# Kernel optimization log

Measured on AMD Instinct MI355X. Metric: run time of the kernel, lower is better.

The kernel has to match this reference:

```python
import jax, jax.numpy as jnp
import numpy as np

B, S, D_MODEL, H, N_LAYERS = 4, 1024, 512, 8, 6
DEPTH = D_MODEL // H


def setup_inputs() -> dict:
    key = jax.random.key(0)
    ks = jax.random.split(key, 16)
    sc = 1.0 / np.sqrt(D_MODEL)
    inp = {
        'v': jax.random.normal(ks[0], (B, S, D_MODEL), jnp.float32),
        'q': jax.random.normal(ks[1], (B, S, D_MODEL), jnp.float32),
        'k': jax.random.normal(ks[2], (B, S, D_MODEL), jnp.float32),
        'wq_w': jax.random.normal(ks[3], (D_MODEL, D_MODEL), jnp.float32) * sc,
        'wq_b': jnp.zeros((D_MODEL,), jnp.float32),
        'wk_w': jax.random.normal(ks[4], (D_MODEL, D_MODEL), jnp.float32) * sc,
        'wk_b': jnp.zeros((D_MODEL,), jnp.float32),
        'wv_w': jax.random.normal(ks[5], (D_MODEL, D_MODEL), jnp.float32) * sc,
        'wv_b': jnp.zeros((D_MODEL,), jnp.float32),
        'wo_w': jax.random.normal(ks[6], (D_MODEL, D_MODEL), jnp.float32) * sc,
        'wo_b': jnp.zeros((D_MODEL,), jnp.float32),
        'aug_hb': jax.random.uniform(ks[7], (N_LAYERS, 1), jnp.float32),
        'aug_pi': jax.random.uniform(ks[8], (N_LAYERS, 1), jnp.float32),
        'aug_at': jax.random.uniform(ks[9], (N_LAYERS, 1), jnp.float32),
        'table_hb': jax.random.normal(ks[10], (S, S), jnp.float32),
        'table_pi': jax.random.normal(ks[11], (S, S), jnp.float32),
        'mask': (jax.random.uniform(ks[12], (B, 1, S, S)) < 0.1).astype(jnp.float32),
        'block_num': 0,
    }
    return inp


def _split_heads(x):
    # (B, S, d_model) -> (B, H, S, depth)
    return x.reshape(B, S, H, DEPTH).transpose(0, 2, 1, 3)


def reference(v, q, k, wq_w, wq_b, wk_w, wk_b, wv_w, wv_b, wo_w, wo_b,
              aug_hb, aug_pi, aug_at, table_hb, table_pi, mask, block_num):
    qh = _split_heads(q @ wq_w + wq_b)
    kh = _split_heads(k @ wk_w + wk_b)
    vh = _split_heads(v @ wv_w + wv_b)

    # NOTE: original call site swaps q/k positionally, so scores = K . Q^T
    scores = jnp.einsum('bhid,bhjd->bhij', kh, qh)  # (B,H,S,S)
    dk = jnp.float32(DEPTH)
    logits = scores / jnp.sqrt(dk) + mask * (-1e9)

    # per-layer table augmentation (tables broadcast over batch & heads)
    logits = logits * aug_at[block_num] \
        + aug_hb[block_num] * table_hb \
        + aug_pi[block_num] * table_pi

    # joint softmax over axes (2, 3)
    m = jnp.max(logits, axis=(2, 3), keepdims=True)
    e = jnp.exp(logits - m)
    attn = e / jnp.sum(e, axis=(2, 3), keepdims=True)

    ctx = jnp.einsum('bhij,bhjd->bhid', attn, vh)          # (B,H,S,depth)
    ctx = ctx.transpose(0, 2, 1, 3).reshape(B, S, D_MODEL)  # concat heads
    out = ctx @ wo_w + wo_b
    return out, attn
```

## Files before the change

### kernel.cpp

```cpp
#include <hip/hip_runtime.h>
#include <math.h>

#define NS 1024
#define DM 512
#define NH 8
#define DEPTH 64

#define OFF_QH   0
#define OFF_KH   2097152
#define OFF_VH   4194304
#define OFF_CTX0 0
#define OFF_CTX1 2097152
#define OFF_PART 6291456

#define ESW(row, col) ((col) ^ ((((row) >> 3) & 7) << 2))

#define LO_SCALE 2048.0f
#define LO_INV   (1.0f/2048.0f)
#define F16_MIN_NORM 6.1035156e-5f
#define ASCALE   4096.0f
#define AUNSCALE (1.0f/4096.0f)

typedef float f4 __attribute__((ext_vector_type(4)));
typedef _Float16 h8 __attribute__((ext_vector_type(8)));
typedef _Float16 h4 __attribute__((ext_vector_type(4)));
typedef float f32x4v __attribute__((ext_vector_type(4)));

#define SPLIT1(x, hi_e, lo_e) {                                          \
    const float x_ = (x);                                                \
    _Float16 t = (fabsf(x_) >= F16_MIN_NORM) ? (_Float16)x_ : (_Float16)0.f; \
    hi_e = t;                                                            \
    lo_e = (_Float16)((x_ - (float)t) * LO_SCALE);                       \
}

#define SPLIT8(u0, u1, hi, lo) {                                         \
    SPLIT1(u0.x, hi[0], lo[0]) SPLIT1(u0.y, hi[1], lo[1])                \
    SPLIT1(u0.z, hi[2], lo[2]) SPLIT1(u0.w, hi[3], lo[3])                \
    SPLIT1(u1.x, hi[4], lo[4]) SPLIT1(u1.y, hi[5], lo[5])                \
    SPLIT1(u1.z, hi[6], lo[6]) SPLIT1(u1.w, hi[7], lo[7])                \
}

#define MM(accH, accM, a_h, a_l, b_h, b_l) {                                   \
    accH = __builtin_amdgcn_mfma_f32_16x16x32_f16(a_h, b_h, accH, 0, 0, 0);    \
    accM = __builtin_amdgcn_mfma_f32_16x16x32_f16(a_l, b_h, accM, 0, 0, 0);    \
    accM = __builtin_amdgcn_mfma_f32_16x16x32_f16(a_h, b_l, accM, 0, 0, 0);    \
}
#define MM1(acc, a_h, a_l, b_h, b_l) {                                         \
    acc = __builtin_amdgcn_mfma_f32_16x16x32_f16(a_h, b_h, acc, 0, 0, 0);      \
    acc = __builtin_amdgcn_mfma_f32_16x16x32_f16(a_l, b_h, acc, 0, 0, 0);      \
    acc = __builtin_amdgcn_mfma_f32_16x16x32_f16(a_h, b_l, acc, 0, 0, 0);      \
}

__device__ __forceinline__ void prep_one(
    const float* __restrict__ W, _Float16* __restrict__ whi,
    _Float16* __restrict__ wlo, int g)
{
    const int kk = g >> 7;
    const int n  = (g & 127) * 4;
    const float4 f = *(const float4*)(W + (size_t)kk * DM + n);
    const int gbase = (kk >> 3) * 128 + (kk & 7);
    #define PREP1(val, nn) {                                             \
        const int a_ = ((nn) >> 4) * 8192 + gbase + ((nn) & 15) * 8;     \
        _Float16 h_; _Float16 l_;                                        \
        SPLIT1(val, h_, l_)                                              \
        whi[a_] = h_; wlo[a_] = l_;                                      \
    }
    PREP1(f.x, n + 0) PREP1(f.y, n + 1) PREP1(f.z, n + 2) PREP1(f.w, n + 3)
    #undef PREP1
}

__global__ __launch_bounds__(256) void k_prep_qkv(
    const float* __restrict__ wq, const float* __restrict__ wk,
    const float* __restrict__ wv, float* __restrict__ attn)
{
    const int w = blockIdx.y;
    const float* W = (w == 0) ? wq : (w == 1) ? wk : wv;
    _Float16* base = (_Float16*)attn + (size_t)w * 524288;
    prep_one(W, base, base + 262144, blockIdx.x * 256 + threadIdx.x);
}

__global__ __launch_bounds__(256) void k_prep_wo(
    const float* __restrict__ wo, float* __restrict__ ws)
{
    _Float16* base = (_Float16*)(ws + OFF_VH);
    prep_one(wo, base, base + 262144, blockIdx.x * 256 + threadIdx.x);
}

__global__ __launch_bounds__(256) void k_prep_aux(
    const float* __restrict__ mask, const float* __restrict__ t_hb,
    const float* __restrict__ t_pi,
    const float* __restrict__ aug_hb, const float* __restrict__ aug_pi,
    const float* __restrict__ aug_at, const int* __restrict__ bnum,
    float* __restrict__ outp)
{
    const int g = blockIdx.x * 256 + threadIdx.x;
    const size_t e0 = (size_t)g * 4;
    const size_t t0 = e0 & (size_t)(NS*NS - 1);
    const int bn = bnum[0];
    const float at = aug_at[bn], hb = aug_hb[bn], pi = aug_pi[bn];
    const float m_at = -1e9f * at;
    const f4 m4 = *(const f4*)(mask + e0);
    const f4 th = *(const f4*)(t_hb + t0);
    const f4 tp = *(const f4*)(t_pi + t0);
    h4 o;
    float a;
    a = fmaf(m4.x, m_at, fmaf(hb, th.x, pi*tp.x)); if (a < -60000.f) a = -60000.f; o[0] = (_Float16)a;
    a = fmaf(m4.y, m_at, fmaf(hb, th.y, pi*tp.y)); if (a < -60000.f) a = -60000.f; o[1] = (_Float16)a;
    a = fmaf(m4.z, m_at, fmaf(hb, th.z, pi*tp.z)); if (a < -60000.f) a = -60000.f; o[2] = (_Float16)a;
    a = fmaf(m4.w, m_at, fmaf(hb, th.w, pi*tp.w)); if (a < -60000.f) a = -60000.f; o[3] = (_Float16)a;
    *(h4*)((_Float16*)outp + e0) = o;
}

__global__ __launch_bounds__(256, 3) void k_proj(
    const float* __restrict__ q, const float* __restrict__ k, const float* __restrict__ v,
    const float* __restrict__ bq, const float* __restrict__ bk, const float* __restrict__ bv,
    float* __restrict__ ws, const float* __restrict__ attn)
{
    const float *X, *bias; int wsel;
    if (blockIdx.z == 0)      { X=q; bias=bq; wsel=0; }
    else if (blockIdx.z == 1) { X=k; bias=bk; wsel=1; }
    else                      { X=v; bias=bv; wsel=2; }
    float* outf = ws + OFF_VH;
    _Float16* outh = (_Float16*)(ws + (wsel == 0 ? OFF_QH : OFF_KH));

    const int f = blockIdx.x + (blockIdx.y << 3);
    const int n0 = (f >> 5) * 64, m0 = (f & 31) * 128;
    const int tid = threadIdx.x, l = tid & 63, w = tid >> 6;
    const int lr = l & 15, lg = l >> 4;

    const _Float16* whi = (const _Float16*)attn + (size_t)wsel * 524288;
    const _Float16* wlo = whi + 262144;
    const float* ap0 = X + (size_t)(m0 + w*32 + lr) * DM + lg*8;
    const float* ap1 = ap0 + (size_t)16 * DM;
    const _Float16* bh_base = whi + (size_t)(n0 >> 4) * 8192 + lg*128 + lr*8;
    const _Float16* bl_base = wlo + (size_t)(n0 >> 4) * 8192 + lg*128 + lr*8;

    f32x4v aH00 = 0, aH01 = 0, aH02 = 0, aH03 = 0;
    f32x4v aH10 = 0, aH11 = 0, aH12 = 0, aH13 = 0;
    f32x4v aM00 = 0, aM01 = 0, aM02 = 0, aM03 = 0;
    f32x4v aM10 = 0, aM11 = 0, aM12 = 0, aM13 = 0;

    #pragma unroll 1
    for (int kb = 0; kb < DM; kb += 32) {
        h8 ah0, al0, ah1, al1;
        {
            const float4 u0 = *(const float4*)(ap0 + kb);
            const float4 u1 = *(const float4*)(ap0 + kb + 4);
            SPLIT8(u0, u1, ah0, al0);
            const float4 v0 = *(const float4*)(ap1 + kb);
            const float4 v1 = *(const float4*)(ap1 + kb + 4);
            SPLIT8(v0, v1, ah1, al1);
        }
        const int boff = kb * 16;
        const h8 bh0 = *(const h8*)(bh_base + boff);
        const h8 bh1 = *(const h8*)(bh_base + boff + 8192);
        const h8 bh2 = *(const h8*)(bh_base + boff + 16384);
        const h8 bh3 = *(const h8*)(bh_base + boff + 24576);
        const h8 bl0 = *(const h8*)(bl_base + boff);
        const h8 bl1 = *(const h8*)(bl_base + boff + 8192);
        const h8 bl2 = *(const h8*)(bl_base + boff + 16384);
        const h8 bl3 = *(const h8*)(bl_base + boff + 24576);

        MM(aH00, aM00, ah0, al0, bh0, bl0) MM(aH01, aM01, ah0, al0, bh1, bl1)
        MM(aH02, aM02, ah0, al0, bh2, bl2) MM(aH03, aM03, ah0, al0, bh3, bl3)
        MM(aH10, aM10, ah1, al1, bh0, bl0) MM(aH11, aM11, ah1, al1, bh1, bl1)
        MM(aH12, aM12, ah1, al1, bh2, bl2) MM(aH13, aM13, ah1, al1, bh3, bl3)
    }

    const int h = n0 >> 6;
    #define STORE_TILE(accH, accM, nt, mt) {                                 \
        const int n = n0 + (nt)*16 + lr;                                     \
        const float bsv = bias[n];                                           \
        const int d = n & 63;                                                \
        const int mbase = m0 + w*32 + (mt)*16 + lg*4;                        \
        _Pragma("unroll")                                                    \
        for (int r = 0; r < 4; ++r) {                                        \
            const int m = mbase + r;                                         \
            const int bb = m >> 10, s = m & 1023;                            \
            const float val = fmaf(accM[r], LO_INV, accH[r]) + bsv;          \
            if (wsel == 2) {                                                 \
                outf[(((size_t)(bb*NH + h))*NS + s)*DEPTH + d] = val;        \
            } else {                                                         \
                _Float16* p = outh + (size_t)(bb*NH + h)*131072              \
                                   + (size_t)s*64 + d;                       \
                const _Float16 hi_ = (_Float16)val;                          \
                p[0]     = hi_;                                              \
                p[65536] = (_Float16)(val - (float)hi_);                     \
            }                                                                \
        }                                                                    \
    }
    STORE_TILE(aH00, aM00, 0, 0) STORE_TILE(aH10, aM10, 0, 1)
    STORE_TILE(aH01, aM01, 1, 0) STORE_TILE(aH11, aM11, 1, 1)
    STORE_TILE(aH02, aM02, 2, 0) STORE_TILE(aH12, aM12, 2, 1)
    STORE_TILE(aH03, aM03, 3, 0) STORE_TILE(aH13, aM13, 3, 1)
    #undef STORE_TILE
}

__global__ __launch_bounds__(256, 4) void k_score(
    float* __restrict__ ws,
    const _Float16* __restrict__ aux,
    const float* __restrict__ aug_at, const int* __restrict__ bnum,
    float* __restrict__ attn)
{
    __shared__ float wred[4];
    const int bh = blockIdx.z, b = bh >> 3;
    const int f = blockIdx.x + (blockIdx.y << 3);
    const int r = f & 7, qq = f >> 3;
    const int it = ((r & 1) << 2) | (qq & 3);
    const int jt_ = ((r >> 1) << 1) | (qq >> 2);
    const int i0 = it * 128, j0 = jt_ * 128;
    const _Float16* kb_ = (const _Float16*)(ws + OFF_KH) + (size_t)bh * 131072;
    const _Float16* qb_ = (const _Float16*)(ws + OFF_QH) + (size_t)bh * 131072;
    const int tid = threadIdx.x, l = tid & 63, w = tid >> 6;
    const int lr = l & 15, lg = l >> 4;

    const _Float16* ka = kb_ + (size_t)(i0 + w*32 + lr) * 64 + lg*8;
    const _Float16* qa = qb_ + (size_t)(j0 + lr) * 64 + lg*8;

    f32x4v acc[2][8] = {};
    #pragma unroll
    for (int d0 = 0; d0 < 2; ++d0) {
        const int dd = d0 * 32;
        const h8 ah0 = *(const h8*)(ka + dd);
        const h8 al0 = *(const h8*)(ka + dd + 65536);
        const h8 ah1 = *(const h8*)(ka + dd + 16*64);
        const h8 al1 = *(const h8*)(ka + dd + 16*64 + 65536);
        #pragma unroll
        for (int jt = 0; jt < 8; ++jt) {
            const h8 bhf = *(const h8*)(qa + dd + jt*16*64);
            const h8 blf = *(const h8*)(qa + dd + jt*16*64 + 65536);
            MM1(acc[0][jt], ah0, al0, bhf, blf)
            MM1(acc[1][jt], ah1, al1, bhf, blf)
        }
    }

    const int bn = bnum[0];
    const float sc_at = 0.125f * aug_at[bn];
    float local = 0.f;
    #pragma unroll
    for (int it2 = 0; it2 < 2; ++it2) {
        #pragma unroll
        for (int rr = 0; rr < 4; ++rr) {
            const int gi = i0 + w*32 + it2*16 + lg*4 + rr;
            const size_t xrow = ((size_t)b*NS + gi)*NS;
            const size_t arow = ((size_t)bh*NS + gi)*NS;
            #pragma unroll
            for (int jt = 0; jt < 8; ++jt) {
                const int gj = j0 + jt*16 + lr;
                const float xv = (float)aux[xrow + gj];
                const float e = __expf(fmaf(acc[it2][jt][rr], sc_at, xv));
                attn[arow + gj] = e;
                local += e;
            }
        }
    }
    #pragma unroll
    for (int o = 32; o > 0; o >>= 1) local += __shfl_down(local, o);
    if ((tid & 63) == 0) wred[tid >> 6] = local;
    __syncthreads();
    if (tid == 0)
        ws[OFF_PART + bh*64 + it*8 + jt_] =
            (wred[0] + wred[1]) + (wred[2] + wred[3]);
}

__global__ __launch_bounds__(256, 4) void k_pv(
    float* __restrict__ ws, float* __restrict__ attn)
{
    __shared__ float Es[64][68];
    __shared__ float Vs[64][68];
    __shared__ float s_inv;
    const int F = blockIdx.x + (blockIdx.y << 1) + (blockIdx.z << 5);
    const int r = F & 7, s = F >> 3;
    const int bh = (r << 2) | (s & 3);
    const int w = s >> 2;
    const int i0 = (w >> 1) * 64;
    const int jh = w & 1;
    const int b = bh >> 3, h = bh & 7;
    const float* vh = ws + OFF_VH + (size_t)bh*NS*DEPTH;
    float* pctx = ws + (jh ? OFF_CTX1 : OFF_CTX0);
    const int tid = threadIdx.x, tx = tid & 15, ty = tid >> 4;
    const int er_ = tid >> 4, ec4 = tid & 15;

    if (tid < 64) {
        float vsum = ws[OFF_PART + bh*64 + tid];
        #pragma unroll
        for (int o = 32; o > 0; o >>= 1) vsum += __shfl_down(vsum, o);
        if (tid == 0) s_inv = 1.0f / vsum;
    }
    __syncthreads();
    const float inv = s_inv;

    float acc[4][4] = {};
    for (int jt = 0; jt < 8; ++jt) {
        const int j0 = jh*512 + jt*64;
        #pragma unroll
        for (int l = 0; l < 4; ++l) {
            const int rr = er_ + l*16;
            float* ap = attn + ((size_t)bh*NS + i0 + rr)*NS + j0 + ec4*4;
            f4 e4 = *(const f4*)ap;
            e4 *= inv;
            *(f4*)ap = e4;
            Es[ec4*4+0][ESW(ec4*4+0, rr)] = e4.x;
            Es[ec4*4+1][ESW(ec4*4+1, rr)] = e4.y;
            Es[ec4*4+2][ESW(ec4*4+2, rr)] = e4.z;
            Es[ec4*4+3][ESW(ec4*4+3, rr)] = e4.w;
            *(float4*)&Vs[rr][ec4*4] = *(const float4*)(vh + (size_t)(j0+rr)*DEPTH + ec4*4);
        }
        __syncthreads();
        #pragma unroll
        for (int jj = 0; jj < 64; ++jj) {
            const float4 a  = *(const float4*)&Es[jj][ESW(jj, ty*4)];
            const float4 vv = *(const float4*)&Vs[jj][tx*4];
            const float av[4] = {a.x,a.y,a.z,a.w};
            const float vw[4] = {vv.x,vv.y,vv.z,vv.w};
            #pragma unroll
            for (int i = 0; i < 4; ++i)
                #pragma unroll
                for (int d = 0; d < 4; ++d)
                    acc[i][d] = fmaf(av[i], vw[d], acc[i][d]);
        }
        __syncthreads();
    }
    #pragma unroll
    for (int i = 0; i < 4; ++i) {
        const int gi = i0 + ty*4 + i;
        float4 o;
        o.x = acc[i][0]; o.y = acc[i][1]; o.z = acc[i][2]; o.w = acc[i][3];
        *(float4*)(pctx + ((size_t)b*NS + gi)*DM + h*DEPTH + tx*4) = o;
    }
}

__global__ __launch_bounds__(256, 3) void k_out(
    const float* __restrict__ wsc, const float* __restrict__ bo,
    float* __restrict__ outp)
{
    const int f = blockIdx.x + (blockIdx.y << 3);
    const int n0 = (f >> 5) * 64, m0 = (f & 31) * 128;
    const int tid = threadIdx.x, l = tid & 63, w = tid >> 6;
    const int lr = l & 15, lg = l >> 4;

    const _Float16* whi = (const _Float16*)(wsc + OFF_VH);
    const _Float16* wlo = whi + 262144;
    const float* ap0 = wsc + OFF_CTX0 + (size_t)(m0 + w*32 + lr) * DM + lg*8;
    const float* ap1 = wsc + OFF_CTX1 + (size_t)(m0 + w*32 + lr) * DM + lg*8;
    const _Float16* bh_base = whi + (size_t)(n0 >> 4) * 8192 + lg*128 + lr*8;
    const _Float16* bl_base = wlo + (size_t)(n0 >> 4) * 8192 + lg*128 + lr*8;

    f32x4v aH00 = 0, aH01 = 0, aH02 = 0, aH03 = 0;
    f32x4v aH10 = 0, aH11 = 0, aH12 = 0, aH13 = 0;
    f32x4v aM00 = 0, aM01 = 0, aM02 = 0, aM03 = 0;
    f32x4v aM10 = 0, aM11 = 0, aM12 = 0, aM13 = 0;

    #pragma unroll 1
    for (int kb = 0; kb < DM; kb += 32) {
        h8 ah0, al0, ah1, al1;
        {
            float4 u0 = *(const float4*)(ap0 + kb);
            float4 u1 = *(const float4*)(ap0 + kb + 4);
            const float4 c0 = *(const float4*)(ap1 + kb);
            const float4 c1 = *(const float4*)(ap1 + kb + 4);
            u0.x=(u0.x+c0.x)*ASCALE; u0.y=(u0.y+c0.y)*ASCALE;
            u0.z=(u0.z+c0.z)*ASCALE; u0.w=(u0.w+c0.w)*ASCALE;
            u1.x=(u1.x+c1.x)*ASCALE; u1.y=(u1.y+c1.y)*ASCALE;
            u1.z=(u1.z+c1.z)*ASCALE; u1.w=(u1.w+c1.w)*ASCALE;
            SPLIT8(u0, u1, ah0, al0);
            float4 v0 = *(const float4*)(ap0 + (size_t)16*DM + kb);
            float4 v1 = *(const float4*)(ap0 + (size_t)16*DM + kb + 4);
            const float4 d0 = *(const float4*)(ap1 + (size_t)16*DM + kb);
            const float4 d1 = *(const float4*)(ap1 + (size_t)16*DM + kb + 4);
            v0.x=(v0.x+d0.x)*ASCALE; v0.y=(v0.y+d0.y)*ASCALE;
            v0.z=(v0.z+d0.z)*ASCALE; v0.w=(v0.w+d0.w)*ASCALE;
            v1.x=(v1.x+d1.x)*ASCALE; v1.y=(v1.y+d1.y)*ASCALE;
            v1.z=(v1.z+d1.z)*ASCALE; v1.w=(v1.w+d1.w)*ASCALE;
            SPLIT8(v0, v1, ah1, al1);
        }
        const int boff = kb * 16;
        const h8 bh0 = *(const h8*)(bh_base + boff);
        const h8 bh1 = *(const h8*)(bh_base + boff + 8192);
        const h8 bh2 = *(const h8*)(bh_base + boff + 16384);
        const h8 bh3 = *(const h8*)(bh_base + boff + 24576);
        const h8 bl0 = *(const h8*)(bl_base + boff);
        const h8 bl1 = *(const h8*)(bl_base + boff + 8192);
        const h8 bl2 = *(const h8*)(bl_base + boff + 16384);
        const h8 bl3 = *(const h8*)(bl_base + boff + 24576);

        MM(aH00, aM00, ah0, al0, bh0, bl0) MM(aH01, aM01, ah0, al0, bh1, bl1)
        MM(aH02, aM02, ah0, al0, bh2, bl2) MM(aH03, aM03, ah0, al0, bh3, bl3)
        MM(aH10, aM10, ah1, al1, bh0, bl0) MM(aH11, aM11, ah1, al1, bh1, bl1)
        MM(aH12, aM12, ah1, al1, bh2, bl2) MM(aH13, aM13, ah1, al1, bh3, bl3)
    }

    #define STORE_TILE(accH, accM, nt, mt) {                                 \
        const int n = n0 + (nt)*16 + lr;                                     \
        const float bsv = bo[n];                                             \
        const int mbase = m0 + w*32 + (mt)*16 + lg*4;                        \
        _Pragma("unroll")                                                    \
        for (int r = 0; r < 4; ++r)                                          \
            outp[(size_t)(mbase + r)*DM + n] =                               \
                fmaf(accM[r], LO_INV, accH[r]) * AUNSCALE + bsv;             \
    }
    STORE_TILE(aH00, aM00, 0, 0) STORE_TILE(aH10, aM10, 0, 1)
    STORE_TILE(aH01, aM01, 1, 0) STORE_TILE(aH11, aM11, 1, 1)
    STORE_TILE(aH02, aM02, 2, 0) STORE_TILE(aH12, aM12, 2, 1)
    STORE_TILE(aH03, aM03, 3, 0) STORE_TILE(aH13, aM13, 3, 1)
    #undef STORE_TILE
}

extern "C" void kernel_launch(void* const* d_in, const int* in_sizes, int n_in,
                              void* d_out, int out_size, void* d_ws, size_t ws_size,
                              hipStream_t stream)
{
    const float* v    = (const float*)d_in[0];
    const float* q    = (const float*)d_in[1];
    const float* k    = (const float*)d_in[2];
    const float* wq_w = (const float*)d_in[3];
    const float* wq_b = (const float*)d_in[4];
    const float* wk_w = (const float*)d_in[5];
    const float* wk_b = (const float*)d_in[6];
    const float* wv_w = (const float*)d_in[7];
    const float* wv_b = (const float*)d_in[8];
    const float* wo_w = (const float*)d_in[9];
    const float* wo_b = (const float*)d_in[10];
    const float* aug_hb = (const float*)d_in[11];
    const float* aug_pi = (const float*)d_in[12];
    const float* aug_at = (const float*)d_in[13];
    const float* t_hb   = (const float*)d_in[14];
    const float* t_pi   = (const float*)d_in[15];
    const float* mask   = (const float*)d_in[16];
    const int*   bnum   = (const int*)d_in[17];

    float* ws   = (float*)d_ws;
    float* outp = (float*)d_out;
    float* attn = (float*)d_out + (size_t)4*NS*DM;

    hipLaunchKernelGGL(k_prep_qkv, dim3(256, 3), dim3(256), 0, stream,
                       wq_w, wk_w, wv_w, attn);
    hipLaunchKernelGGL(k_prep_aux, dim3(4096), dim3(256), 0, stream,
                       mask, t_hb, t_pi, aug_hb, aug_pi, aug_at, bnum, outp);
    hipLaunchKernelGGL(k_proj, dim3(8, 32, 3), dim3(256), 0, stream,
                       q, k, v, wq_b, wk_b, wv_b, ws, attn);
    hipLaunchKernelGGL(k_score, dim3(8, 8, 32), dim3(256), 0, stream,
                       ws, (const _Float16*)outp, aug_at, bnum, attn);
    hipLaunchKernelGGL(k_pv, dim3(2, 16, 32), dim3(256), 0, stream, ws, attn);
    hipLaunchKernelGGL(k_prep_wo, dim3(256, 1), dim3(256), 0, stream, wo_w, ws);
    hipLaunchKernelGGL(k_out, dim3(8, 32), dim3(256), 0, stream,
                       ws, wo_b, outp);
}
```

Baseline: 222.5 us.

## Recompute scores in PV kernel instead of round-tripping unnormalized attn

The score kernel now only computes exp-sums for the softmax denominator and no longer writes unnormalized exponentials to the attention output. The PV kernel recomputes QK^T tiles with split-fp16 MFMA, applies the augmentation and exp, normalizes, then writes attn once and feeds the values to shared memory. This removes a full read and write pass over the 128 MB attention tensor, in exchange for computing the score matmul and exp twice. Context buffers move to new workspace offsets so the Q/K halves stay intact for recomputation.

```diff
diff --git a/kernel.cpp b/kernel.cpp
--- a/kernel.cpp
+++ b/kernel.cpp
@@ -9,9 +9,9 @@
 #define OFF_QH   0
 #define OFF_KH   2097152
 #define OFF_VH   4194304
-#define OFF_CTX0 0
-#define OFF_CTX1 2097152
 #define OFF_PART 6291456
+#define OFF_CTXA 6295552
+#define OFF_CTXB 8392704
 
 #define ESW(row, col) ((col) ^ ((((row) >> 3) & 7) << 2))
 
@@ -199,8 +199,7 @@
 __global__ __launch_bounds__(256, 4) void k_score(
     float* __restrict__ ws,
     const _Float16* __restrict__ aux,
-    const float* __restrict__ aug_at, const int* __restrict__ bnum,
-    float* __restrict__ attn)
+    const float* __restrict__ aug_at, const int* __restrict__ bnum)
 {
     __shared__ float wred[4];
     const int bh = blockIdx.z, b = bh >> 3;
@@ -243,14 +242,11 @@
         for (int rr = 0; rr < 4; ++rr) {
             const int gi = i0 + w*32 + it2*16 + lg*4 + rr;
             const size_t xrow = ((size_t)b*NS + gi)*NS;
-            const size_t arow = ((size_t)bh*NS + gi)*NS;
             #pragma unroll
             for (int jt = 0; jt < 8; ++jt) {
                 const int gj = j0 + jt*16 + lr;
                 const float xv = (float)aux[xrow + gj];
-                const float e = __expf(fmaf(acc[it2][jt][rr], sc_at, xv));
-                attn[arow + gj] = e;
-                local += e;
+                local += __expf(fmaf(acc[it2][jt][rr], sc_at, xv));
             }
         }
     }
@@ -264,7 +260,10 @@
 }
 
 __global__ __launch_bounds__(256, 4) void k_pv(
-    float* __restrict__ ws, float* __restrict__ attn)
+    float* __restrict__ ws,
+    const _Float16* __restrict__ aux,
+    const float* __restrict__ aug_at, const int* __restrict__ bnum,
+    float* __restrict__ attn)
 {
     __shared__ float Es[64][68];
     __shared__ float Vs[64][68];
@@ -277,9 +276,13 @@
     const int jh = w & 1;
     const int b = bh >> 3, h = bh & 7;
     const float* vh = ws + OFF_VH + (size_t)bh*NS*DEPTH;
-    float* pctx = ws + (jh ? OFF_CTX1 : OFF_CTX0);
+    const _Float16* kb_ = (const _Float16*)(ws + OFF_KH) + (size_t)bh * 131072;
+    const _Float16* qb_ = (const _Float16*)(ws + OFF_QH) + (size_t)bh * 131072;
+    float* pctx = ws + (jh ? OFF_CTXB : OFF_CTXA);
     const int tid = threadIdx.x, tx = tid & 15, ty = tid >> 4;
     const int er_ = tid >> 4, ec4 = tid & 15;
+    const int l = tid & 63, wv = tid >> 6;
+    const int lr = l & 15, lg = l >> 4;
 
     if (tid < 64) {
         float vsum = ws[OFF_PART + bh*64 + tid];
@@ -289,23 +292,54 @@
     }
     __syncthreads();
     const float inv = s_inv;
+    const int bn = bnum[0];
+    const float sc_at = 0.125f * aug_at[bn];
+
+    const _Float16* ka = kb_ + (size_t)(i0 + wv*16 + lr) * 64 + lg*8;
 
     float acc[4][4] = {};
     for (int jt = 0; jt < 8; ++jt) {
         const int j0 = jh*512 + jt*64;
         #pragma unroll
-        for (int l = 0; l < 4; ++l) {
-            const int rr = er_ + l*16;
-            float* ap = attn + ((size_t)bh*NS + i0 + rr)*NS + j0 + ec4*4;
-            f4 e4 = *(const f4*)ap;
-            e4 *= inv;
-            *(f4*)ap = e4;
-            Es[ec4*4+0][ESW(ec4*4+0, rr)] = e4.x;
-            Es[ec4*4+1][ESW(ec4*4+1, rr)] = e4.y;
-            Es[ec4*4+2][ESW(ec4*4+2, rr)] = e4.z;
-            Es[ec4*4+3][ESW(ec4*4+3, rr)] = e4.w;
+        for (int l4 = 0; l4 < 4; ++l4) {
+            const int rr = er_ + l4*16;
             *(float4*)&Vs[rr][ec4*4] = *(const float4*)(vh + (size_t)(j0+rr)*DEPTH + ec4*4);
         }
+        const _Float16* qa = qb_ + (size_t)(j0 + lr) * 64 + lg*8;
+        f32x4v sa0 = 0, sa1 = 0, sa2 = 0, sa3 = 0;
+        #pragma unroll
+        for (int d0 = 0; d0 < 2; ++d0) {
+            const int dd = d0 * 32;
+            const h8 ah = *(const h8*)(ka + dd);
+            const h8 al = *(const h8*)(ka + dd + 65536);
+            const h8 b0h = *(const h8*)(qa + dd);
+            const h8 b0l = *(const h8*)(qa + dd + 65536);
+            const h8 b1h = *(const h8*)(qa + dd + 16*64);
+            const h8 b1l = *(const h8*)(qa + dd + 16*64 + 65536);
+            const h8 b2h = *(const h8*)(qa + dd + 32*64);
+            const h8 b2l = *(const h8*)(qa + dd + 32*64 + 65536);
+            const h8 b3h = *(const h8*)(qa + dd + 48*64);
+            const h8 b3l = *(const h8*)(qa + dd + 48*64 + 65536);
+            MM1(sa0, ah, al, b0h, b0l)
+            MM1(sa1, ah, al, b1h, b1l)
+            MM1(sa2, ah, al, b2h, b2l)
+            MM1(sa3, ah, al, b3h, b3l)
+        }
+        #define PTILE(sa, jt16) {                                              \
+            const int jloc = (jt16)*16 + lr;                                   \
+            const int gj = j0 + jloc;                                          \
+            _Pragma("unroll")                                                  \
+            for (int rr = 0; rr < 4; ++rr) {                                   \
+                const int iloc = wv*16 + lg*4 + rr;                            \
+                const int gi = i0 + iloc;                                      \
+                const float xv = (float)aux[((size_t)b*NS + gi)*NS + gj];      \
+                const float P = __expf(fmaf(sa[rr], sc_at, xv)) * inv;         \
+                attn[((size_t)bh*NS + gi)*NS + gj] = P;                        \
+                Es[jloc][ESW(jloc, iloc)] = P;                                 \
+            }                                                                  \
+        }
+        PTILE(sa0, 0) PTILE(sa1, 1) PTILE(sa2, 2) PTILE(sa3, 3)
+        #undef PTILE
         __syncthreads();
         #pragma unroll
         for (int jj = 0; jj < 64; ++jj) {
@@ -341,8 +375,8 @@
 
     const _Float16* whi = (const _Float16*)(wsc + OFF_VH);
     const _Float16* wlo = whi + 262144;
-    const float* ap0 = wsc + OFF_CTX0 + (size_t)(m0 + w*32 + lr) * DM + lg*8;
-    const float* ap1 = wsc + OFF_CTX1 + (size_t)(m0 + w*32 + lr) * DM + lg*8;
+    const float* ap0 = wsc + OFF_CTXA + (size_t)(m0 + w*32 + lr) * DM + lg*8;
+    const float* ap1 = wsc + OFF_CTXB + (size_t)(m0 + w*32 + lr) * DM + lg*8;
     const _Float16* bh_base = whi + (size_t)(n0 >> 4) * 8192 + lg*128 + lr*8;
     const _Float16* bl_base = wlo + (size_t)(n0 >> 4) * 8192 + lg*128 + lr*8;
 
@@ -440,8 +474,9 @@
     hipLaunchKernelGGL(k_proj, dim3(8, 32, 3), dim3(256), 0, stream,
                        q, k, v, wq_b, wk_b, wv_b, ws, attn);
     hipLaunchKernelGGL(k_score, dim3(8, 8, 32), dim3(256), 0, stream,
+                       ws, (const _Float16*)outp, aug_at, bnum);
+    hipLaunchKernelGGL(k_pv, dim3(2, 16, 32), dim3(256), 0, stream,
                        ws, (const _Float16*)outp, aug_at, bnum, attn);
-    hipLaunchKernelGGL(k_pv, dim3(2, 16, 32), dim3(256), 0, stream, ws, attn);
     hipLaunchKernelGGL(k_prep_wo, dim3(256, 1), dim3(256), 0, stream, wo_w, ws);
     hipLaunchKernelGGL(k_out, dim3(8, 32), dim3(256), 0, stream,
                        ws, wo_b, outp);
```

New measurement: 243.8 us. +9.6%, slower.
